# Performance work log

Hardware: AMD Instinct MI355X
Metric: run time of the kernel (lower is better)

Reference implementation:

```python
import jax, jax.numpy as jnp
import numpy as np

N_NODES = 50000
N_EDGES = 500000
D_IN = 128
HID = 128
N_GRAPHS = 256


def setup_inputs() -> dict:
    key = jax.random.key(0)
    ks = jax.random.split(key, 10)
    x = jax.random.normal(ks[0], (N_NODES, D_IN), dtype=jnp.float32)
    edge_index = jax.random.randint(ks[1], (2, N_EDGES), 0, N_NODES, dtype=jnp.int64)
    batch = jnp.sort(jax.random.randint(ks[2], (N_NODES,), 0, N_GRAPHS, dtype=jnp.int64))
    s = 1.0 / np.sqrt(D_IN)
    W1_rel = jax.random.uniform(ks[3], (HID, D_IN), jnp.float32, -s, s)
    W1_root = jax.random.uniform(ks[4], (HID, D_IN), jnp.float32, -s, s)
    b1 = jnp.zeros((HID,), jnp.float32)
    s2 = 1.0 / np.sqrt(HID)
    W2_rel = jax.random.uniform(ks[5], (HID, HID), jnp.float32, -s2, s2)
    W2_root = jax.random.uniform(ks[6], (HID, HID), jnp.float32, -s2, s2)
    b2 = jnp.zeros((HID,), jnp.float32)
    W_out = jax.random.uniform(ks[7], (1, HID), jnp.float32, -s2, s2)
    b_out = jnp.zeros((1,), jnp.float32)
    return {"x": x, "edge_index": edge_index, "batch": batch,
            "W1_rel": W1_rel, "W1_root": W1_root, "b1": b1,
            "W2_rel": W2_rel, "W2_root": W2_root, "b2": b2,
            "W_out": W_out, "b_out": b_out}


def _graph_conv(h, src, dst, W_rel, W_root, b):
    # gather neighbor feats at edge sources, sum-aggregate at destinations
    agg = jax.ops.segment_sum(h[src], dst, num_segments=N_NODES)  # [N, d]
    return agg @ W_rel.T + h @ W_root.T + b


def reference(x, edge_index, batch, W1_rel, W1_root, b1, W2_rel, W2_root, b2, W_out, b_out):
    src, dst = edge_index[0], edge_index[1]
    h = jax.nn.relu(_graph_conv(x, src, dst, W1_rel, W1_root, b1))
    h = jax.nn.relu(_graph_conv(h, src, dst, W2_rel, W2_root, b2))
    # global mean pool per graph
    sums = jax.ops.segment_sum(h, batch, num_segments=N_GRAPHS)  # [G, HID]
    cnts = jax.ops.segment_sum(jnp.ones((N_NODES,), h.dtype), batch, num_segments=N_GRAPHS)
    pooled = sums / jnp.maximum(cnts, 1.0)[:, None]
    return pooled @ W_out.T + b_out  # [G, 1]
```

## Files before the change

### kernel.cpp

```cpp
#include <hip/hip_runtime.h>
#include <hip/hip_bf16.h>

#define N_NODES  50000
#define N_EDGES  500000
#define DIM      128
#define N_GRAPHS 256

#define SCAN_B   512
#define SCAN_NB  ((N_NODES + SCAN_B - 1) / SCAN_B)

#define WSTRIDE  264

typedef __attribute__((ext_vector_type(8))) short bf16x8;
typedef __attribute__((ext_vector_type(4))) float f32x4;

__device__ __forceinline__ unsigned short f2bf(float f) {
    __hip_bfloat16 h = __float2bfloat16(f);
    return *(unsigned short*)&h;
}
__device__ __forceinline__ float bflo(unsigned int v) {
    unsigned int u = v << 16; return __uint_as_float(u);
}
__device__ __forceinline__ float bfhi(unsigned int v) {
    unsigned int u = v & 0xffff0000u; return __uint_as_float(u);
}

__global__ void cvt_kernel(const float* __restrict__ in, unsigned short* __restrict__ out)
{
    int i = blockIdx.x * blockDim.x + threadIdx.x;
    float4 v = ((const float4*)in)[i];
    ushort4 o;
    o.x = f2bf(v.x); o.y = f2bf(v.y); o.z = f2bf(v.z); o.w = f2bf(v.w);
    ((ushort4*)out)[i] = o;
}

__global__ void hist_kernel(const int* __restrict__ dst, int* __restrict__ deg)
{
    int e = blockIdx.x * blockDim.x + threadIdx.x;
    if (e < N_EDGES) atomicAdd(&deg[dst[e]], 1);
}

__global__ __launch_bounds__(SCAN_B)
void block_sum_kernel(const int* __restrict__ deg, int* __restrict__ bsum)
{
    __shared__ int red[SCAN_B];
    int t = threadIdx.x;
    int idx = blockIdx.x * SCAN_B + t;
    red[t] = (idx < N_NODES) ? deg[idx] : 0;
    __syncthreads();
    for (int off = SCAN_B / 2; off > 0; off >>= 1) {
        if (t < off) red[t] += red[t + off];
        __syncthreads();
    }
    if (t == 0) bsum[blockIdx.x] = red[0];
}

__global__ __launch_bounds__(128)
void scan_sums_kernel(int* __restrict__ bsum)
{
    __shared__ int s[128];
    int t = threadIdx.x;
    int v = (t < SCAN_NB) ? bsum[t] : 0;
    s[t] = v;
    __syncthreads();
    for (int off = 1; off < 128; off <<= 1) {
        int u = (t >= off) ? s[t - off] : 0;
        __syncthreads();
        s[t] += u;
        __syncthreads();
    }
    if (t < SCAN_NB) bsum[t] = s[t] - v;
}

__global__ __launch_bounds__(SCAN_B)
void scan_apply_kernel(const int* __restrict__ deg, const int* __restrict__ bsum,
                       int* __restrict__ row_ptr, int* __restrict__ cursor)
{
    __shared__ int s[SCAN_B];
    int t = threadIdx.x;
    int idx = blockIdx.x * SCAN_B + t;
    int v = (idx < N_NODES) ? deg[idx] : 0;
    s[t] = v;
    __syncthreads();
    for (int off = 1; off < SCAN_B; off <<= 1) {
        int u = (t >= off) ? s[t - off] : 0;
        __syncthreads();
        s[t] += u;
        __syncthreads();
    }
    if (idx < N_NODES) {
        int ex = bsum[blockIdx.x] + s[t] - v;
        row_ptr[idx] = ex;
        cursor[idx]  = ex;
    }
    if (idx == 0) row_ptr[N_NODES] = N_EDGES;
}

__global__ void build_kernel(const int* __restrict__ src, const int* __restrict__ dst,
                             int* __restrict__ cursor, int* __restrict__ edge_src)
{
    int e = blockIdx.x * blockDim.x + threadIdx.x;
    if (e < N_EDGES) {
        int pos = atomicAdd(&cursor[dst[e]], 1);
        edge_src[pos] = src[e];
    }
}

__global__ __launch_bounds__(256)
void gather_kernel(const unsigned short* __restrict__ feat,
                   const int* __restrict__ row_ptr,
                   const int* __restrict__ edge_src,
                   unsigned short* __restrict__ agg)
{
    int wid  = (blockIdx.x * blockDim.x + threadIdx.x) >> 6;
    int lane = threadIdx.x & 63;
    int node = __builtin_amdgcn_readfirstlane(wid);

    const unsigned int* f = (const unsigned int*)feat;
    int e  = row_ptr[node];
    int e1 = row_ptr[node + 1];

    float a0 = 0.f, a1 = 0.f, b0 = 0.f, b1 = 0.f;
    for (; e + 1 < e1; e += 2) {
        int sa = edge_src[e], sb = edge_src[e + 1];
        unsigned int va = f[sa * 64 + lane];
        unsigned int vb = f[sb * 64 + lane];
        a0 += bflo(va); a1 += bfhi(va);
        b0 += bflo(vb); b1 += bfhi(vb);
    }
    if (e < e1) {
        unsigned int va = f[edge_src[e] * 64 + lane];
        a0 += bflo(va); a1 += bfhi(va);
    }
    unsigned int o = (unsigned int)f2bf(a0 + b0) | ((unsigned int)f2bf(a1 + b1) << 16);
    ((unsigned int*)agg)[node * 64 + lane] = o;
}

template <bool POOL>
__global__ __launch_bounds__(256)
void gemm_mfma(const unsigned short* __restrict__ Aagg,
               const unsigned short* __restrict__ Ax,
               const float* __restrict__ Wrel, const float* __restrict__ Wroot,
               const float* __restrict__ bias,
               unsigned short* __restrict__ Hout,
               float* __restrict__ pooled,
               const int* __restrict__ batch)
{
    __shared__ __align__(16) unsigned short wlds[128][WSTRIDE];

    const int t = threadIdx.x;

    {
        int col = t >> 1;
        const float* Wm = (t & 1) ? Wroot : Wrel;
        const float4* w4 = (const float4*)(Wm + col * 128);
        unsigned short* dstp = &wlds[col][(t & 1) * 128];
#pragma unroll
        for (int i = 0; i < 32; ++i) {
            float4 v = w4[i];
            ushort4 o;
            o.x = f2bf(v.x); o.y = f2bf(v.y); o.z = f2bf(v.z); o.w = f2bf(v.w);
            *(ushort4*)&dstp[i * 4] = o;
        }
    }
    __syncthreads();

    const int wave = t >> 6;
    const int lane = t & 63;
    const int q    = lane >> 4;
    const int ln15 = lane & 15;
    const int m0   = blockIdx.x * 64 + wave * 16;
    int arow = m0 + ln15;
    int rowc = arow < N_NODES ? arow : N_NODES - 1;

    const unsigned short* A0 = Aagg + (size_t)rowc * DIM + q * 8;
    const unsigned short* A1 = Ax   + (size_t)rowc * DIM + q * 8;

    f32x4 acc[8];
#pragma unroll
    for (int ct = 0; ct < 8; ++ct) acc[ct] = (f32x4){0.f, 0.f, 0.f, 0.f};

#pragma unroll
    for (int ks = 0; ks < 8; ++ks) {
        const unsigned short* ap = (ks < 4) ? (A0 + ks * 32) : (A1 + (ks - 4) * 32);
        bf16x8 afrag = *(const bf16x8*)ap;
        const int k0 = ks * 32;
#pragma unroll
        for (int ct = 0; ct < 8; ++ct) {
            bf16x8 bfrag = *(const bf16x8*)&wlds[ct * 16 + ln15][k0 + q * 8];
            acc[ct] = __builtin_amdgcn_mfma_f32_16x16x32_bf16(afrag, bfrag, acc[ct], 0, 0, 0);
        }
    }

    float bj[8];
#pragma unroll
    for (int ct = 0; ct < 8; ++ct) bj[ct] = bias[ct * 16 + ln15];

    const int rb = m0 + q * 4;

    if (!POOL) {
#pragma unroll
        for (int ct = 0; ct < 8; ++ct) {
            int coln = ct * 16 + ln15;
#pragma unroll
            for (int r = 0; r < 4; ++r) {
                int row = rb + r;
                if (row < N_NODES) {
                    float v = acc[ct][r] + bj[ct];
                    v = v > 0.f ? v : 0.f;
                    Hout[(size_t)row * DIM + coln] = f2bf(v);
                }
            }
        }
    } else {
        int gg[4];
#pragma unroll
        for (int r = 0; r < 4; ++r) gg[r] = (rb + r < N_NODES) ? batch[rb + r] : -1;
        bool uni = (gg[0] == gg[3]) && (gg[3] >= 0);
#pragma unroll
        for (int ct = 0; ct < 8; ++ct) {
            int coln = ct * 16 + ln15;
            float v[4];
#pragma unroll
            for (int r = 0; r < 4; ++r) {
                float x = acc[ct][r] + bj[ct];
                v[r] = x > 0.f ? x : 0.f;
            }
            if (uni) {
                atomicAdd(&pooled[gg[0] * DIM + coln], v[0] + v[1] + v[2] + v[3]);
            } else {
#pragma unroll
                for (int r = 0; r < 4; ++r)
                    if (gg[r] >= 0) atomicAdd(&pooled[gg[r] * DIM + coln], v[r]);
            }
        }
    }
}

__global__ void finalize_kernel(const float* __restrict__ pooled, const int* __restrict__ batch,
                                const float* __restrict__ Wout, const float* __restrict__ bout,
                                float* __restrict__ out)
{
    int g = blockIdx.x;
    int lane = threadIdx.x;

    int lo0 = 0, hi0 = N_NODES;
    while (lo0 < hi0) { int m = (lo0 + hi0) >> 1; if (batch[m] < g) lo0 = m + 1; else hi0 = m; }
    int lo1 = lo0, hi1 = N_NODES;
    while (lo1 < hi1) { int m = (lo1 + hi1) >> 1; if (batch[m] < g + 1) lo1 = m + 1; else hi1 = m; }
    int cnt = lo1 - lo0;

    float s = pooled[g * DIM + lane]      * Wout[lane]
            + pooled[g * DIM + 64 + lane] * Wout[64 + lane];
#pragma unroll
    for (int off = 32; off > 0; off >>= 1) s += __shfl_xor(s, off, 64);
    if (lane == 0) {
        float c = (float)(cnt > 1 ? cnt : 1);
        out[g] = s / c + bout[0];
    }
}

extern "C" void kernel_launch(void* const* d_in, const int* in_sizes, int n_in,
                              void* d_out, int out_size, void* d_ws, size_t ws_size,
                              hipStream_t stream)
{
    const float* x       = (const float*)d_in[0];
    const int*   ei      = (const int*)d_in[1];
    const int*   batch   = (const int*)d_in[2];
    const float* W1_rel  = (const float*)d_in[3];
    const float* W1_root = (const float*)d_in[4];
    const float* b1      = (const float*)d_in[5];
    const float* W2_rel  = (const float*)d_in[6];
    const float* W2_root = (const float*)d_in[7];
    const float* b2      = (const float*)d_in[8];
    const float* W_out   = (const float*)d_in[9];
    const float* b_out   = (const float*)d_in[10];
    float* out = (float*)d_out;

    const int* src  = ei;
    const int* dstv = ei + N_EDGES;

    char* ws = (char*)d_ws;
    unsigned short* aggb = (unsigned short*)ws;
    unsigned short* xb   = (unsigned short*)(ws + 12800000);
    unsigned short* h1b  = (unsigned short*)(ws + 25600000);
    float* pooled        = (float*)(ws + 38400000);
    int*   deg           = (int*)  (ws + 38531072);
    int*   row_ptr       = (int*)  (ws + 38731072);
    int*   edge_src      = (int*)  (ws + 38931200);
    int*   cursor        = (int*)  (ws + 40931200);
    int*   bsum          = (int*)  (ws + 41131200);

    hipMemsetAsync(deg, 0, N_NODES * sizeof(int), stream);
    hipMemsetAsync(pooled, 0, N_GRAPHS * DIM * sizeof(float), stream);
    cvt_kernel       <<<(N_NODES * DIM / 4) / 256, 256, 0, stream>>>(x, xb);
    hist_kernel      <<<(N_EDGES + 255) / 256, 256, 0, stream>>>(dstv, deg);
    block_sum_kernel <<<SCAN_NB, SCAN_B, 0, stream>>>(deg, bsum);
    scan_sums_kernel <<<1, 128, 0, stream>>>(bsum);
    scan_apply_kernel<<<SCAN_NB, SCAN_B, 0, stream>>>(deg, bsum, row_ptr, cursor);
    build_kernel     <<<(N_EDGES + 255) / 256, 256, 0, stream>>>(src, dstv, cursor, edge_src);

    const int gemm_grid = (N_NODES + 63) / 64;

    gather_kernel<<<N_NODES / 4, 256, 0, stream>>>(xb, row_ptr, edge_src, aggb);
    gemm_mfma<false><<<gemm_grid, 256, 0, stream>>>(
        aggb, xb, W1_rel, W1_root, b1, h1b, nullptr, nullptr);

    gather_kernel<<<N_NODES / 4, 256, 0, stream>>>(h1b, row_ptr, edge_src, aggb);
    gemm_mfma<true><<<gemm_grid, 256, 0, stream>>>(
        aggb, h1b, W2_rel, W2_root, b2, nullptr, pooled, batch);

    finalize_kernel<<<N_GRAPHS, 64, 0, stream>>>(pooled, batch, W_out, b_out, out);
}
```

Measured before the change: 275.5 us.

## Pre-convert weights to bf16 fragment layout, double GEMM rows per block, unroll gather

```diff
diff --git a/kernel.cpp b/kernel.cpp
--- a/kernel.cpp
+++ b/kernel.cpp
@@ -9,8 +9,6 @@
 #define SCAN_B   512
 #define SCAN_NB  ((N_NODES + SCAN_B - 1) / SCAN_B)
 
-#define WSTRIDE  264
-
 typedef __attribute__((ext_vector_type(8))) short bf16x8;
 typedef __attribute__((ext_vector_type(4))) float f32x4;
 
@@ -18,12 +16,8 @@
     __hip_bfloat16 h = __float2bfloat16(f);
     return *(unsigned short*)&h;
 }
-__device__ __forceinline__ float bflo(unsigned int v) {
-    unsigned int u = v << 16; return __uint_as_float(u);
-}
-__device__ __forceinline__ float bfhi(unsigned int v) {
-    unsigned int u = v & 0xffff0000u; return __uint_as_float(u);
-}
+__device__ __forceinline__ float bflo(unsigned int v) { return __uint_as_float(v << 16); }
+__device__ __forceinline__ float bfhi(unsigned int v) { return __uint_as_float(v & 0xffff0000u); }
 
 __global__ void cvt_kernel(const float* __restrict__ in, unsigned short* __restrict__ out)
 {
@@ -32,6 +26,29 @@
     ushort4 o;
     o.x = f2bf(v.x); o.y = f2bf(v.y); o.z = f2bf(v.z); o.w = f2bf(v.w);
     ((ushort4*)out)[i] = o;
+}
+
+__global__ __launch_bounds__(256)
+void wcvt_kernel(const float* __restrict__ W1_rel, const float* __restrict__ W1_root,
+                 const float* __restrict__ W2_rel, const float* __restrict__ W2_root,
+                 unsigned short* __restrict__ Wb)
+{
+    int u = blockIdx.x * blockDim.x + threadIdx.x;
+    int layer = u >> 12;
+    int kb    = (u >> 7) & 31;
+    int col   = u & 127;
+    int k0    = kb * 8;
+    const float* Wrel  = layer ? W2_rel  : W1_rel;
+    const float* Wroot = layer ? W2_root : W1_root;
+    const float* srcp = (k0 < 128) ? (Wrel + col * 128 + k0) : (Wroot + col * 128 + (k0 - 128));
+    float4 v0 = ((const float4*)srcp)[0];
+    float4 v1 = ((const float4*)srcp)[1];
+    ushort4 o0, o1;
+    o0.x = f2bf(v0.x); o0.y = f2bf(v0.y); o0.z = f2bf(v0.z); o0.w = f2bf(v0.w);
+    o1.x = f2bf(v1.x); o1.y = f2bf(v1.y); o1.z = f2bf(v1.z); o1.w = f2bf(v1.w);
+    unsigned short* dst = Wb + (size_t)layer * 32768 + ((kb * 128 + col) * 8);
+    ((ushort4*)dst)[0] = o0;
+    ((ushort4*)dst)[1] = o1;
 }
 
 __global__ void hist_kernel(const int* __restrict__ dst, int* __restrict__ deg)
@@ -120,19 +137,27 @@
     int e  = row_ptr[node];
     int e1 = row_ptr[node + 1];
 
-    float a0 = 0.f, a1 = 0.f, b0 = 0.f, b1 = 0.f;
-    for (; e + 1 < e1; e += 2) {
-        int sa = edge_src[e], sb = edge_src[e + 1];
-        unsigned int va = f[sa * 64 + lane];
-        unsigned int vb = f[sb * 64 + lane];
-        a0 += bflo(va); a1 += bfhi(va);
-        b0 += bflo(vb); b1 += bfhi(vb);
-    }
-    if (e < e1) {
+    float s0 = 0.f, s1 = 0.f, t0 = 0.f, t1 = 0.f;
+    float u0 = 0.f, u1 = 0.f, w0 = 0.f, w1 = 0.f;
+    for (; e + 3 < e1; e += 4) {
+        int ia = edge_src[e],     ib = edge_src[e + 1];
+        int ic = edge_src[e + 2], id = edge_src[e + 3];
+        unsigned int va = f[ia * 64 + lane];
+        unsigned int vb = f[ib * 64 + lane];
+        unsigned int vc = f[ic * 64 + lane];
+        unsigned int vd = f[id * 64 + lane];
+        s0 += bflo(va); s1 += bfhi(va);
+        t0 += bflo(vb); t1 += bfhi(vb);
+        u0 += bflo(vc); u1 += bfhi(vc);
+        w0 += bflo(vd); w1 += bfhi(vd);
+    }
+    for (; e < e1; ++e) {
         unsigned int va = f[edge_src[e] * 64 + lane];
-        a0 += bflo(va); a1 += bfhi(va);
-    }
-    unsigned int o = (unsigned int)f2bf(a0 + b0) | ((unsigned int)f2bf(a1 + b1) << 16);
+        s0 += bflo(va); s1 += bfhi(va);
+    }
+    float lo = (s0 + t0) + (u0 + w0);
+    float hi = (s1 + t1) + (u1 + w1);
+    unsigned int o = (unsigned int)f2bf(lo) | ((unsigned int)f2bf(hi) << 16);
     ((unsigned int*)agg)[node * 64 + lane] = o;
 }
 
@@ -140,28 +165,21 @@
 __global__ __launch_bounds__(256)
 void gemm_mfma(const unsigned short* __restrict__ Aagg,
                const unsigned short* __restrict__ Ax,
-               const float* __restrict__ Wrel, const float* __restrict__ Wroot,
+               const unsigned short* __restrict__ Wb,
                const float* __restrict__ bias,
                unsigned short* __restrict__ Hout,
                float* __restrict__ pooled,
                const int* __restrict__ batch)
 {
-    __shared__ __align__(16) unsigned short wlds[128][WSTRIDE];
+    __shared__ __align__(16) unsigned short wlds[32768];
 
     const int t = threadIdx.x;
 
     {
-        int col = t >> 1;
-        const float* Wm = (t & 1) ? Wroot : Wrel;
-        const float4* w4 = (const float4*)(Wm + col * 128);
-        unsigned short* dstp = &wlds[col][(t & 1) * 128];
-#pragma unroll
-        for (int i = 0; i < 32; ++i) {
-            float4 v = w4[i];
-            ushort4 o;
-            o.x = f2bf(v.x); o.y = f2bf(v.y); o.z = f2bf(v.z); o.w = f2bf(v.w);
-            *(ushort4*)&dstp[i * 4] = o;
-        }
+        const uint4* s4 = (const uint4*)Wb;
+        uint4* d4 = (uint4*)wlds;
+#pragma unroll
+        for (int i = 0; i < 16; ++i) d4[t + i * 256] = s4[t + i * 256];
     }
     __syncthreads();
 
@@ -169,26 +187,35 @@
     const int lane = t & 63;
     const int q    = lane >> 4;
     const int ln15 = lane & 15;
-    const int m0   = blockIdx.x * 64 + wave * 16;
-    int arow = m0 + ln15;
-    int rowc = arow < N_NODES ? arow : N_NODES - 1;
-
-    const unsigned short* A0 = Aagg + (size_t)rowc * DIM + q * 8;
-    const unsigned short* A1 = Ax   + (size_t)rowc * DIM + q * 8;
-
-    f32x4 acc[8];
-#pragma unroll
-    for (int ct = 0; ct < 8; ++ct) acc[ct] = (f32x4){0.f, 0.f, 0.f, 0.f};
+    const int m0   = blockIdx.x * 128 + wave * 16;
+
+    int r0 = m0 + ln15;      int r0c = r0 < N_NODES ? r0 : N_NODES - 1;
+    int r1 = m0 + 64 + ln15; int r1c = r1 < N_NODES ? r1 : N_NODES - 1;
+
+    const unsigned short* A00 = Aagg + (size_t)r0c * DIM + q * 8;
+    const unsigned short* A01 = Ax   + (size_t)r0c * DIM + q * 8;
+    const unsigned short* A10 = Aagg + (size_t)r1c * DIM + q * 8;
+    const unsigned short* A11 = Ax   + (size_t)r1c * DIM + q * 8;
+
+    f32x4 acc0[8], acc1[8];
+#pragma unroll
+    for (int ct = 0; ct < 8; ++ct) {
+        acc0[ct] = (f32x4){0.f, 0.f, 0.f, 0.f};
+        acc1[ct] = (f32x4){0.f, 0.f, 0.f, 0.f};
+    }
 
 #pragma unroll
     for (int ks = 0; ks < 8; ++ks) {
-        const unsigned short* ap = (ks < 4) ? (A0 + ks * 32) : (A1 + (ks - 4) * 32);
-        bf16x8 afrag = *(const bf16x8*)ap;
-        const int k0 = ks * 32;
+        const unsigned short* p0 = (ks < 4) ? (A00 + ks * 32) : (A01 + (ks - 4) * 32);
+        const unsigned short* p1 = (ks < 4) ? (A10 + ks * 32) : (A11 + (ks - 4) * 32);
+        bf16x8 a0 = *(const bf16x8*)p0;
+        bf16x8 a1 = *(const bf16x8*)p1;
+        const unsigned short* wrow = wlds + (ks * 4 + q) * 1024;
 #pragma unroll
         for (int ct = 0; ct < 8; ++ct) {
-            bf16x8 bfrag = *(const bf16x8*)&wlds[ct * 16 + ln15][k0 + q * 8];
-            acc[ct] = __builtin_amdgcn_mfma_f32_16x16x32_bf16(afrag, bfrag, acc[ct], 0, 0, 0);
+            bf16x8 bf = *(const bf16x8*)&wrow[(ct * 16 + ln15) * 8];
+            acc0[ct] = __builtin_amdgcn_mfma_f32_16x16x32_bf16(a0, bf, acc0[ct], 0, 0, 0);
+            acc1[ct] = __builtin_amdgcn_mfma_f32_16x16x32_bf16(a1, bf, acc1[ct], 0, 0, 0);
         }
     }
 
@@ -196,42 +223,46 @@
 #pragma unroll
     for (int ct = 0; ct < 8; ++ct) bj[ct] = bias[ct * 16 + ln15];
 
-    const int rb = m0 + q * 4;
-
-    if (!POOL) {
-#pragma unroll
-        for (int ct = 0; ct < 8; ++ct) {
-            int coln = ct * 16 + ln15;
-#pragma unroll
-            for (int r = 0; r < 4; ++r) {
-                int row = rb + r;
-                if (row < N_NODES) {
-                    float v = acc[ct][r] + bj[ct];
-                    v = v > 0.f ? v : 0.f;
-                    Hout[(size_t)row * DIM + coln] = f2bf(v);
+#pragma unroll
+    for (int rt = 0; rt < 2; ++rt) {
+        const f32x4* acc = rt ? acc1 : acc0;
+        const int rb = m0 + rt * 64 + q * 4;
+
+        if (!POOL) {
+#pragma unroll
+            for (int ct = 0; ct < 8; ++ct) {
+                int coln = ct * 16 + ln15;
+#pragma unroll
+                for (int r = 0; r < 4; ++r) {
+                    int row = rb + r;
+                    if (row < N_NODES) {
+                        float v = acc[ct][r] + bj[ct];
+                        v = v > 0.f ? v : 0.f;
+                        Hout[(size_t)row * DIM + coln] = f2bf(v);
+                    }
                 }
             }
-        }
-    } else {
-        int gg[4];
-#pragma unroll
-        for (int r = 0; r < 4; ++r) gg[r] = (rb + r < N_NODES) ? batch[rb + r] : -1;
-        bool uni = (gg[0] == gg[3]) && (gg[3] >= 0);
-#pragma unroll
-        for (int ct = 0; ct < 8; ++ct) {
-            int coln = ct * 16 + ln15;
-            float v[4];
-#pragma unroll
-            for (int r = 0; r < 4; ++r) {
-                float x = acc[ct][r] + bj[ct];
-                v[r] = x > 0.f ? x : 0.f;
-            }
-            if (uni) {
-                atomicAdd(&pooled[gg[0] * DIM + coln], v[0] + v[1] + v[2] + v[3]);
-            } else {
-#pragma unroll
-                for (int r = 0; r < 4; ++r)
-                    if (gg[r] >= 0) atomicAdd(&pooled[gg[r] * DIM + coln], v[r]);
+        } else {
+            int gg[4];
+#pragma unroll
+            for (int r = 0; r < 4; ++r) gg[r] = (rb + r < N_NODES) ? batch[rb + r] : -1;
+            bool uni = (gg[0] == gg[3]) && (gg[3] >= 0);
+#pragma unroll
+            for (int ct = 0; ct < 8; ++ct) {
+                int coln = ct * 16 + ln15;
+                float v[4];
+#pragma unroll
+                for (int r = 0; r < 4; ++r) {
+                    float x = acc[ct][r] + bj[ct];
+                    v[r] = x > 0.f ? x : 0.f;
+                }
+                if (uni) {
+                    atomicAdd(&pooled[gg[0] * DIM + coln], v[0] + v[1] + v[2] + v[3]);
+                } else {
+#pragma unroll
+                    for (int r = 0; r < 4; ++r)
+                        if (gg[r] >= 0) atomicAdd(&pooled[gg[r] * DIM + coln], v[r]);
+                }
             }
         }
     }
@@ -290,25 +321,27 @@
     int*   edge_src      = (int*)  (ws + 38931200);
     int*   cursor        = (int*)  (ws + 40931200);
     int*   bsum          = (int*)  (ws + 41131200);
+    unsigned short* Wb   = (unsigned short*)(ws + 41131712);
 
     hipMemsetAsync(deg, 0, N_NODES * sizeof(int), stream);
     hipMemsetAsync(pooled, 0, N_GRAPHS * DIM * sizeof(float), stream);
     cvt_kernel       <<<(N_NODES * DIM / 4) / 256, 256, 0, stream>>>(x, xb);
+    wcvt_kernel      <<<32, 256, 0, stream>>>(W1_rel, W1_root, W2_rel, W2_root, Wb);
     hist_kernel      <<<(N_EDGES + 255) / 256, 256, 0, stream>>>(dstv, deg);
     block_sum_kernel <<<SCAN_NB, SCAN_B, 0, stream>>>(deg, bsum);
     scan_sums_kernel <<<1, 128, 0, stream>>>(bsum);
     scan_apply_kernel<<<SCAN_NB, SCAN_B, 0, stream>>>(deg, bsum, row_ptr, cursor);
     build_kernel     <<<(N_EDGES + 255) / 256, 256, 0, stream>>>(src, dstv, cursor, edge_src);
 
-    const int gemm_grid = (N_NODES + 63) / 64;
+    const int gemm_grid = (N_NODES + 127) / 128;
 
     gather_kernel<<<N_NODES / 4, 256, 0, stream>>>(xb, row_ptr, edge_src, aggb);
     gemm_mfma<false><<<gemm_grid, 256, 0, stream>>>(
-        aggb, xb, W1_rel, W1_root, b1, h1b, nullptr, nullptr);
+        aggb, xb, Wb, b1, h1b, nullptr, nullptr);
 
     gather_kernel<<<N_NODES / 4, 256, 0, stream>>>(h1b, row_ptr, edge_src, aggb);
     gemm_mfma<true><<<gemm_grid, 256, 0, stream>>>(
-        aggb, h1b, W2_rel, W2_root, b2, nullptr, pooled, batch);
+        aggb, h1b, Wb + 32768, b2, nullptr, pooled, batch);
 
     finalize_kernel<<<N_GRAPHS, 64, 0, stream>>>(pooled, batch, W_out, b_out, out);
 }
```

New measurement: 243.5 us. 1.13x faster.
